# Optimization experiments

Hardware: AMD Instinct MI355X
Metric: run time of the kernel (lower is better)

The kernel has to match this reference:

```python
import jax, jax.numpy as jnp
import numpy as np

N = 100000   # nodes
E = 1600000  # edges (avg degree 16)
IN, HID, OUT = 128, 128, 64


def setup_inputs() -> dict:
    key = jax.random.key(0)
    k = jax.random.split(key, 6)
    feat = jax.random.normal(k[0], (N, IN), dtype=jnp.float32)
    src = jax.random.randint(k[1], (E,), 0, N)
    dst = jax.random.randint(k[2], (E,), 0, N)
    W1 = jax.random.normal(k[3], (IN, HID), dtype=jnp.float32) * (1.0 / np.sqrt(IN))
    b1 = jnp.zeros((HID,), dtype=jnp.float32)
    W2 = jax.random.normal(k[4], (HID, OUT), dtype=jnp.float32) * (1.0 / np.sqrt(HID))
    b2 = jnp.zeros((OUT,), dtype=jnp.float32)
    return {"feat": feat, "src": src, "dst": dst, "W1": W1, "b1": b1, "W2": W2, "b2": b2}


def _graph_conv(x, src, dst, c_src, c_dst, W, b):
    # DGL GraphConv, norm='both': D_dst^{-1/2} A (D_src^{-1/2} X W) + b
    # Apply W before the edge gather (mathematically identical, less edge traffic).
    h = (x * c_src[:, None]) @ W                      # [N, out]
    m = jax.ops.segment_sum(h[src], dst, num_segments=N)  # SpMM aggregate
    return m * c_dst[:, None] + b


def reference(feat, src, dst, W1, b1, W2, b2):
    ones = jnp.ones((src.shape[0],), dtype=feat.dtype)
    out_deg = jax.ops.segment_sum(ones, src, num_segments=N)
    in_deg = jax.ops.segment_sum(ones, dst, num_segments=N)
    c_src = jnp.clip(out_deg, 1.0, None) ** -0.5
    c_dst = jnp.clip(in_deg, 1.0, None) ** -0.5
    h = jax.nn.relu(_graph_conv(feat, src, dst, c_src, c_dst, W1, b1))
    h = _graph_conv(h, src, dst, c_src, c_dst, W2, b2)
    # dgl.mean_nodes over a single graph -> [1, OUT]
    return jnp.mean(h, axis=0, keepdims=True)
```

## Files before the change

### kernel.cpp

```cpp
#include <hip/hip_runtime.h>
#include <hip/hip_bf16.h>

#define FD 128
#define OD 64
#define SLOT 64
#define MAXNB 512
#define CHUNK 4096

typedef __hip_bfloat16 bf16;
typedef unsigned int u32;
typedef unsigned short u16;
typedef unsigned char u8;
typedef __attribute__((ext_vector_type(8))) short short8;
typedef __attribute__((ext_vector_type(4))) float f32x4;
typedef __attribute__((ext_vector_type(2))) float f32x2;

__device__ __forceinline__ float ldf(const float* p, size_t i) { return p[i]; }
__device__ __forceinline__ float ldf(const bf16* p, size_t i) { return __bfloat162float(p[i]); }
__device__ __forceinline__ float us2f(u16 u) {
    union { float f; u32 i; } w; w.i = ((u32)u) << 16; return w.f;
}
__device__ __forceinline__ u16 f2us(float f) {
    bf16 h = __float2bfloat16(f);
    return *reinterpret_cast<u16*>(&h);
}

__device__ __forceinline__ u32 f8e(float x) {
    union { float f; u32 i; } w; w.f = x;
    u32 s = (w.i >> 24) & 0x80u;
    float a = fabsf(x);
    if (a < 0.015625f) {
        u32 m = (u32)(int)rintf(a * 512.0f);
        return s | m;
    }
    if (a > 448.0f) a = 448.0f;
    w.f = a;
    u32 mag = w.i + 0x7FFFFu + ((w.i >> 20) & 1u);
    if (mag > 0x43E00000u) mag = 0x43E00000u;
    u32 e8 = (mag >> 23) - 120u;
    u32 m3 = (mag >> 20) & 7u;
    return s | (e8 << 3) | m3;
}
__device__ __forceinline__ float f8d(u32 b) {
    float v;
    if ((b & 0x78u) == 0u) {
        v = (float)(b & 7u) * 0x1p-9f;
    } else {
        union { u32 i; float f; } w;
        w.i = ((b & 0x7Fu) << 20) + 0x3C000000u;
        v = w.f;
    }
    return (b & 0x80u) ? -v : v;
}

__global__ void k_sniff(const u16* w1raw, unsigned* flag) {
    int t = threadIdx.x;
    int insane = 0;
    for (int i = t; i < 128; i += 64) {
        unsigned e = (w1raw[i] >> 7) & 0xFF;
        if (e != 0 && (e < 100 || e > 140)) insane++;
    }
    for (int o = 32; o > 0; o >>= 1) insane += __shfl_down(insane, o);
    if (t == 0) *flag = (insane > 16) ? 1u : 0u;
}

__global__ void k_wtF(const unsigned* __restrict__ flag,
                      const void* __restrict__ W1, const void* __restrict__ b1,
                      u16* __restrict__ W1T, float* __restrict__ b1f) {
    int t = blockIdx.x * 256 + threadIdx.x;
    int nn = t >> 7, k = t & 127;
    if (*flag == 0u) {
        W1T[t] = f2us(ldf((const bf16*)W1, (size_t)k * FD + nn));
        if (blockIdx.x == 0 && threadIdx.x < FD) b1f[threadIdx.x] = ldf((const bf16*)b1, threadIdx.x);
    } else {
        W1T[t] = f2us(ldf((const float*)W1, (size_t)k * FD + nn));
        if (blockIdx.x == 0 && threadIdx.x < FD) b1f[threadIdx.x] = ldf((const float*)b1, threadIdx.x);
    }
}

__global__ void k_f8F(const unsigned* __restrict__ flag,
                      const void* __restrict__ feat, const float* __restrict__ c_src,
                      u32* __restrict__ f8w, int N) {
    long wi = (long)blockIdx.x * 256 + threadIdx.x;
    long nw = (long)(N + 1) * 32;
    if (wi >= nw) return;
    int row = (int)(wi >> 5);
    if (row >= N) { f8w[wi] = 0u; return; }
    float cs = c_src[row];
    size_t b0 = (size_t)wi * 4;
    u32 pk;
    if (*flag == 0u) {
        const bf16* f = (const bf16*)feat;
        pk = f8e(cs * ldf(f, b0))       | (f8e(cs * ldf(f, b0 + 1)) << 8)
           | (f8e(cs * ldf(f, b0 + 2)) << 16) | (f8e(cs * ldf(f, b0 + 3)) << 24);
    } else {
        const float* f = (const float*)feat;
        pk = f8e(cs * ldf(f, b0))       | (f8e(cs * ldf(f, b0 + 1)) << 8)
           | (f8e(cs * ldf(f, b0 + 2)) << 16) | (f8e(cs * ldf(f, b0 + 3)) << 24);
    }
    f8w[wi] = pk;
}

__global__ __launch_bounds__(1024) void k_histC(const int* __restrict__ src,
                                                const int* __restrict__ dst,
                                                u32* __restrict__ cmT_d, u32* __restrict__ cmT_s,
                                                int E, int NB) {
    __shared__ u32 hd[MAXNB], hs[MAXNB];
    int t = threadIdx.x, blk = blockIdx.x;
    for (int i = t; i < NB; i += 1024) { hd[i] = 0; hs[i] = 0; }
    __syncthreads();
    long e0 = (long)blk * CHUNK;
    #pragma unroll
    for (int k = 0; k < CHUNK / 1024; k++) {
        long e = e0 + t + 1024L * k;
        if (e < E) {
            atomicAdd(&hd[((u32)dst[e]) >> 8], 1u);
            atomicAdd(&hs[((u32)src[e]) >> 8], 1u);
        }
    }
    __syncthreads();
    for (int i = t; i < NB; i += 1024) {
        cmT_d[(size_t)blk * NB + i] = hd[i];
        cmT_s[(size_t)blk * NB + i] = hs[i];
    }
}

__global__ __launch_bounds__(256) void k_colpre(u32* __restrict__ cmT_d, u32* __restrict__ cmT_s,
                                                u32* __restrict__ totd, u32* __restrict__ tots,
                                                int NB, int nchunk) {
    __shared__ u32 s[256];
    int bb = blockIdx.x;
    u32* cm = (bb < NB) ? cmT_d : cmT_s;
    u32* tot = (bb < NB) ? totd : tots;
    int b = (bb < NB) ? bb : bb - NB;
    int t = threadIdx.x;
    u32 carry = 0;
    for (int c0 = 0; c0 < nchunk; c0 += 256) {
        int c = c0 + t;
        u32 v = (c < nchunk) ? cm[(size_t)c * NB + b] : 0u;
        s[t] = v;
        __syncthreads();
        for (int o = 1; o < 256; o <<= 1) {
            u32 x = (t >= o) ? s[t - o] : 0u;
            __syncthreads();
            s[t] += x;
            __syncthreads();
        }
        if (c < nchunk) cm[(size_t)c * NB + b] = carry + s[t] - v;
        u32 btot = s[255];
        __syncthreads();
        carry += btot;
    }
    if (t == 0) tot[b] = carry;
}

__global__ void k_scanB(const u32* __restrict__ totd, const u32* __restrict__ tots,
                        u32* __restrict__ bstart_d, u32* __restrict__ bstart_s, int NB) {
    __shared__ u32 ts[1024];
    const u32* h = blockIdx.x ? tots : totd;
    u32* bs = blockIdx.x ? bstart_s : bstart_d;
    int t = threadIdx.x;
    int k = (NB + 1023) / 1024;
    int b0 = t * k;
    u32 s = 0;
    for (int i = 0; i < k; i++) { int b = b0 + i; if (b < NB) s += h[b]; }
    ts[t] = s;
    __syncthreads();
    for (int o = 1; o < 1024; o <<= 1) {
        u32 x = (t >= o) ? ts[t - o] : 0u;
        __syncthreads();
        ts[t] += x;
        __syncthreads();
    }
    u32 run = ts[t] - s;
    for (int i = 0; i < k; i++) {
        int b = b0 + i;
        if (b < NB) { bs[b] = run; run += h[b]; }
    }
}

__global__ __launch_bounds__(1024) void k_scat(const int* __restrict__ src,
                                               const int* __restrict__ dst,
                                               const u32* __restrict__ cmT_d,
                                               const u32* __restrict__ cmT_s,
                                               const u32* __restrict__ bstart_d,
                                               const u32* __restrict__ bstart_s,
                                               u32* __restrict__ pairs, u32* __restrict__ srcb,
                                               int E, int NB) {
    __shared__ u32 hd[MAXNB], hs[MAXNB];
    __shared__ u32 baseD[MAXNB], baseS[MAXNB];
    int t = threadIdx.x, blk = blockIdx.x;
    for (int i = t; i < NB; i += 1024) {
        hd[i] = 0; hs[i] = 0;
        baseD[i] = cmT_d[(size_t)blk * NB + i] + bstart_d[i];
        baseS[i] = cmT_s[(size_t)blk * NB + i] + bstart_s[i];
    }
    __syncthreads();
    long e0 = (long)blk * CHUNK;
    #pragma unroll
    for (int k = 0; k < CHUNK / 1024; k++) {
        long e = e0 + t + 1024L * k;
        if (e < E) {
            u32 s = (u32)src[e], d = (u32)dst[e];
            u32 rd = atomicAdd(&hd[d >> 8], 1u);
            u32 rs = atomicAdd(&hs[s >> 8], 1u);
            pairs[baseD[d >> 8] + rd] = ((d & 255u) << 24) | s;
            srcb [baseS[s >> 8] + rs] = ((s & 255u) << 24) | d;
        }
    }
}

__global__ __launch_bounds__(1024) void k_csr(const u32* __restrict__ pairs,
                                              const u32* __restrict__ bstart,
                                              const u32* __restrict__ bhist, u32* __restrict__ col,
                                              u32* __restrict__ cnt_d, float* __restrict__ c_dst,
                                              int N) {
    __shared__ u32 lc[256];
    int b = blockIdx.x, t = threadIdx.x;
    if (t < 256) lc[t] = 0;
    __syncthreads();
    u32 s0 = bstart[b], c = bhist[b];
    for (u32 i = t; i < c; i += 1024) {
        u32 pk = pairs[s0 + i];
        u32 local = pk >> 24;
        u32 r = atomicAdd(&lc[local], 1u);
        if (r < SLOT) col[(((size_t)b * 256 + local) << 6) + r] = pk & 0xFFFFFFu;
    }
    __syncthreads();
    if (t < 256) {
        int node = b * 256 + t;
        if (node < N) {
            cnt_d[node] = lc[t];
            c_dst[node] = rsqrtf(fmaxf((float)lc[t], 1.0f));
        }
    }
}

__global__ __launch_bounds__(1024) void k_cw(const u32* __restrict__ srcb,
                                             const u32* __restrict__ bstart,
                                             const u32* __restrict__ bhist,
                                             const float* __restrict__ c_dst,
                                             float* __restrict__ c_src, float* __restrict__ wprod,
                                             int N) {
    __shared__ u32 lc[256];
    __shared__ float acc[256];
    int b = blockIdx.x, t = threadIdx.x;
    if (t < 256) { lc[t] = 0; acc[t] = 0.0f; }
    __syncthreads();
    u32 s0 = bstart[b], c = bhist[b];
    for (u32 i = t; i < c; i += 1024) {
        u32 pk = srcb[s0 + i];
        atomicAdd(&lc[pk >> 24], 1u);
        atomicAdd(&acc[pk >> 24], c_dst[pk & 0xFFFFFFu]);
    }
    __syncthreads();
    if (t < 256) {
        int node = b * 256 + t;
        if (node < N) {
            float cs = rsqrtf(fmaxf((float)lc[t], 1.0f));
            c_src[node] = cs;
            wprod[node] = acc[t] * cs;
        }
    }
}

__global__ __launch_bounds__(256) void k_layer1a(const u8* __restrict__ f8,
                                                 const u16* __restrict__ W1T,
                                                 const float* __restrict__ b1f,
                                                 const float* __restrict__ c_dst,
                                                 const unsigned* __restrict__ cnt_d,
                                                 const unsigned* __restrict__ col,
                                                 u32* __restrict__ h1_32, int n) {
    __shared__ __align__(16) u16 xsb[64 * 144];
    __shared__ float b1l[FD];
    __shared__ float cdl[64];
    __shared__ unsigned degl[64];
    int t = threadIdx.x;
    int base = blockIdx.x * 64;

    if (t < FD) b1l[t] = b1f[t];
    if (t < 64) {
        int rr = base + t;
        unsigned cd = (rr < n) ? cnt_d[rr] : 0u;
        cdl[t] = (rr < n) ? c_dst[rr] : 0.0f;
        degl[t] = (cd < SLOT) ? cd : SLOT;
    }
    __syncthreads();

    int w = __builtin_amdgcn_readfirstlane(t >> 6);
    int l = t & 63;
    int m0 = w * 16;
    int q = l >> 4, lm = l & 15;
    int j0 = l * 2;
    unsigned zrow = (unsigned)n;

    for (int g = 0; g < 16; g++) {
        int loc = m0 + g;
        int node = base + loc;
        unsigned degv = degl[loc];
        size_t cb = ((size_t)node) << 6;
        float acc0 = 0.0f, acc1 = 0.0f;
        for (unsigned qq = 0; qq < degv; qq += 16) {
            unsigned lim = degv - qq;
            const unsigned* cp = col + cb + qq;
            uint4 P0 = *(const uint4*)(cp);
            uint4 P1 = *(const uint4*)(cp + 4);
            uint4 P2 = *(const uint4*)(cp + 8);
            uint4 P3 = *(const uint4*)(cp + 12);
            unsigned raw[16] = {P0.x, P0.y, P0.z, P0.w, P1.x, P1.y, P1.z, P1.w,
                                P2.x, P2.y, P2.z, P2.w, P3.x, P3.y, P3.z, P3.w};
            #pragma unroll
            for (int k = 0; k < 16; k++) {
                unsigned sk = __builtin_amdgcn_readfirstlane(raw[k]);
                sk = ((unsigned)k < lim) ? sk : zrow;
                u32 v = (u32)*(const u16*)(f8 + (((size_t)sk) << 7) + j0);
#if __has_builtin(__builtin_amdgcn_cvt_pk_f32_fp8)
                f32x2 dd = __builtin_amdgcn_cvt_pk_f32_fp8((int)v, false);
                acc0 += dd[0];
                acc1 += dd[1];
#else
                acc0 += f8d(v & 0xFFu);
                acc1 += f8d(v >> 8);
#endif
            }
        }
        u32 pk = ((u32)f2us(acc1) << 16) | (u32)f2us(acc0);
        *(u32*)&xsb[loc * 144 + j0] = pk;
    }

    short8 af[4];
    #pragma unroll
    for (int s = 0; s < 4; s++)
        af[s] = *(const short8*)&xsb[(m0 + lm) * 144 + s * 32 + q * 8];

    #pragma unroll 1
    for (int h2 = 0; h2 < 2; h2++) {
        #pragma unroll 1
        for (int tt = 0; tt < 4; tt++) {
            int nglob = h2 * 64 + tt * 16 + lm;
            f32x4 c = {0.0f, 0.0f, 0.0f, 0.0f};
            #pragma unroll
            for (int s = 0; s < 4; s++) {
                short8 bfr = *(const short8*)&W1T[(size_t)nglob * FD + s * 32 + q * 8];
                c = __builtin_amdgcn_mfma_f32_16x16x32_bf16(af[s], bfr, c, 0, 0, 0);
            }
            float bb = b1l[nglob];
            #pragma unroll
            for (int r = 0; r < 4; r++) {
                int loc = m0 + q * 4 + r;
                float hv = fmaxf(c[r] * cdl[loc] + bb, 0.0f);
                xsb[loc * 144 + nglob] = f2us(hv);
            }
        }
    }
    __syncthreads();

    #pragma unroll
    for (int i = 0; i < 16; i++) {
        int widx = t + 256 * i;
        int row = widx >> 6, cw = widx & 63;
        if (base + row < n)
            h1_32[((size_t)(base + row)) * 64 + cw] = *(const u32*)&xsb[row * 144 + cw * 2];
    }
}

__global__ __launch_bounds__(256) void k_l1b(const float* __restrict__ wprod,
                                             const u32* __restrict__ h1_32,
                                             float* __restrict__ accum128, int n) {
    __shared__ float part[4][FD];
    int t = threadIdx.x;
    int j2 = t & 63, sub = t >> 6;
    int per = (n + gridDim.x - 1) / gridDim.x;
    int b0 = blockIdx.x * per;
    int be = min(b0 + per, n);
    float a0 = 0.0f, a1 = 0.0f;
    for (int node = b0 + sub; node < be; node += 4) {
        float w = wprod[node];
        u32 v = h1_32[(size_t)node * 64 + j2];
        a0 += w * us2f((u16)(v & 0xffff));
        a1 += w * us2f((u16)(v >> 16));
    }
    part[sub][2 * j2]     = a0;
    part[sub][2 * j2 + 1] = a1;
    __syncthreads();
    if (t < FD)
        unsafeAtomicAdd(&accum128[t], part[0][t] + part[1][t] + part[2][t] + part[3][t]);
}

__global__ void k_finalF(const unsigned* __restrict__ flag,
                         const float* __restrict__ accum128,
                         const void* __restrict__ W2, const void* __restrict__ b2v,
                         void* __restrict__ out, float invN) {
    int j = threadIdx.x;
    float acc = 0.0f;
    if (*flag == 0u) {
        const bf16* w = (const bf16*)W2;
        for (int k = 0; k < FD; k++) acc += accum128[k] * ldf(w, (size_t)k * OD + j);
        ((bf16*)out)[j] = __float2bfloat16(acc * invN + ldf((const bf16*)b2v, j));
    } else {
        const float* w = (const float*)W2;
        for (int k = 0; k < FD; k++) acc += accum128[k] * ldf(w, (size_t)k * OD + j);
        ((float*)out)[j] = acc * invN + ldf((const float*)b2v, j);
    }
}

extern "C" void kernel_launch(void* const* d_in, const int* in_sizes, int n_in,
                              void* d_out, int out_size, void* d_ws, size_t ws_size,
                              hipStream_t stream) {
    const int* src = (const int*)d_in[1];
    const int* dst = (const int*)d_in[2];
    int N = in_sizes[0] / FD;
    int E = in_sizes[1];
    int NB = (N + 255) >> 8;
    int nchunk = (E + CHUNK - 1) / CHUNK;

    char* ws = (char*)d_ws;
    size_t o = 0;
    auto take = [&](size_t bytes) { size_t r = o; o = (o + bytes + 255) & ~(size_t)255; return r; };
    unsigned* flag     = (unsigned*)(ws + take(4096));
    float*    accum128 = (float*)   (ws + take(4096));
    u32*      totd     = (u32*)     (ws + take((size_t)NB * 4));
    u32*      tots     = (u32*)     (ws + take((size_t)NB * 4));
    u32*      bstart_d = (u32*)     (ws + take((size_t)NB * 4));
    u32*      bstart_s = (u32*)     (ws + take((size_t)NB * 4));
    float*    wprod    = (float*)   (ws + take((size_t)N * 4));
    float*    c_src    = (float*)   (ws + take((size_t)N * 4));
    float*    c_dst    = (float*)   (ws + take((size_t)N * 4));
    unsigned* cnt_d    = (unsigned*)(ws + take((size_t)N * 4));
    u16*      W1T      = (u16*)     (ws + take(FD * FD * 2));
    float*    b1f      = (float*)   (ws + take(FD * 4));
    u32*      cmT_d    = (u32*)     (ws + take((size_t)NB * nchunk * 4));
    u32*      cmT_s    = (u32*)     (ws + take((size_t)NB * nchunk * 4));
    size_t scrE = take((((size_t)E * 8) > ((size_t)N * 256)) ? ((size_t)E * 8) : ((size_t)N * 256));
    u32*      pairs    = (u32*)(ws + scrE);
    u32*      srcb     = pairs + E;
    u32*      h1_32    = (u32*)(ws + scrE);
    unsigned* col      = (unsigned*)(ws + take((size_t)N * SLOT * 4));
    u8*       f8       = (u8*)      (ws + take(((size_t)N + 1) * FD));

    hipMemsetAsync(accum128, 0, 4096, stream);

    k_sniff<<<1, 64, 0, stream>>>((const u16*)d_in[3], flag);
    k_wtF<<<64, 256, 0, stream>>>(flag, d_in[3], d_in[4], W1T, b1f);

    k_histC<<<nchunk, 1024, 0, stream>>>(src, dst, cmT_d, cmT_s, E, NB);
    k_colpre<<<2 * NB, 256, 0, stream>>>(cmT_d, cmT_s, totd, tots, NB, nchunk);
    k_scanB<<<2, 1024, 0, stream>>>(totd, tots, bstart_d, bstart_s, NB);
    k_scat<<<nchunk, 1024, 0, stream>>>(src, dst, cmT_d, cmT_s, bstart_d, bstart_s,
                                        pairs, srcb, E, NB);
    k_csr<<<NB, 1024, 0, stream>>>(pairs, bstart_d, totd, col, cnt_d, c_dst, N);
    k_cw<<<NB, 1024, 0, stream>>>(srcb, bstart_s, tots, c_dst, c_src, wprod, N);

    long nw8 = (long)(N + 1) * 32;
    k_f8F<<<(int)((nw8 + 255) / 256), 256, 0, stream>>>(flag, d_in[0], c_src, (u32*)f8, N);

    int gl1 = (N + 63) / 64;
    k_layer1a<<<gl1, 256, 0, stream>>>(f8, W1T, b1f, c_dst, cnt_d, col, h1_32, N);

    k_l1b<<<512, 256, 0, stream>>>(wprod, h1_32, accum128, N);

    float invN = 1.0f / (float)N;
    k_finalF<<<1, 64, 0, stream>>>(flag, accum128, d_in[5], d_in[6], d_out, invN);
}
```

Before: 264.0 us.

## Fuse preprocessing kernels and fold layer-1 reduction into the aggregation kernel

Merges the dtype-sniff, weight transpose and histogram kernels into one launch. The FP8 feature quantisation moves into the c_src kernel, and the accumulator memset into the block scan. The weighted column reduction that k_l1b did is now done inside k_layer1a with shuffles and a per-block atomic, so the bf16 h1 intermediate is never written to or read from global memory. This removes several launches and a full N×128 round trip. In exchange, the dtype sniff is recomputed in every block, and the block scan assumes NB ≤ 1024.

```diff
diff --git a/kernel.cpp b/kernel.cpp
--- a/kernel.cpp
+++ b/kernel.cpp
@@ -53,60 +53,42 @@
     return (b & 0x80u) ? -v : v;
 }
 
-__global__ void k_sniff(const u16* w1raw, unsigned* flag) {
-    int t = threadIdx.x;
-    int insane = 0;
-    for (int i = t; i < 128; i += 64) {
-        unsigned e = (w1raw[i] >> 7) & 0xFF;
-        if (e != 0 && (e < 100 || e > 140)) insane++;
-    }
-    for (int o = 32; o > 0; o >>= 1) insane += __shfl_down(insane, o);
-    if (t == 0) *flag = (insane > 16) ? 1u : 0u;
-}
-
-__global__ void k_wtF(const unsigned* __restrict__ flag,
-                      const void* __restrict__ W1, const void* __restrict__ b1,
-                      u16* __restrict__ W1T, float* __restrict__ b1f) {
-    int t = blockIdx.x * 256 + threadIdx.x;
-    int nn = t >> 7, k = t & 127;
-    if (*flag == 0u) {
-        W1T[t] = f2us(ldf((const bf16*)W1, (size_t)k * FD + nn));
-        if (blockIdx.x == 0 && threadIdx.x < FD) b1f[threadIdx.x] = ldf((const bf16*)b1, threadIdx.x);
-    } else {
-        W1T[t] = f2us(ldf((const float*)W1, (size_t)k * FD + nn));
-        if (blockIdx.x == 0 && threadIdx.x < FD) b1f[threadIdx.x] = ldf((const float*)b1, threadIdx.x);
-    }
-}
-
-__global__ void k_f8F(const unsigned* __restrict__ flag,
-                      const void* __restrict__ feat, const float* __restrict__ c_src,
-                      u32* __restrict__ f8w, int N) {
-    long wi = (long)blockIdx.x * 256 + threadIdx.x;
-    long nw = (long)(N + 1) * 32;
-    if (wi >= nw) return;
-    int row = (int)(wi >> 5);
-    if (row >= N) { f8w[wi] = 0u; return; }
-    float cs = c_src[row];
-    size_t b0 = (size_t)wi * 4;
-    u32 pk;
-    if (*flag == 0u) {
-        const bf16* f = (const bf16*)feat;
-        pk = f8e(cs * ldf(f, b0))       | (f8e(cs * ldf(f, b0 + 1)) << 8)
-           | (f8e(cs * ldf(f, b0 + 2)) << 16) | (f8e(cs * ldf(f, b0 + 3)) << 24);
-    } else {
-        const float* f = (const float*)feat;
-        pk = f8e(cs * ldf(f, b0))       | (f8e(cs * ldf(f, b0 + 1)) << 8)
-           | (f8e(cs * ldf(f, b0 + 2)) << 16) | (f8e(cs * ldf(f, b0 + 3)) << 24);
-    }
-    f8w[wi] = pk;
-}
-
-__global__ __launch_bounds__(1024) void k_histC(const int* __restrict__ src,
-                                                const int* __restrict__ dst,
-                                                u32* __restrict__ cmT_d, u32* __restrict__ cmT_s,
-                                                int E, int NB) {
-    __shared__ u32 hd[MAXNB], hs[MAXNB];
-    int t = threadIdx.x, blk = blockIdx.x;
+__device__ __forceinline__ u32 sniff(const u16* __restrict__ w1raw, u32* shflag) {
+    if (threadIdx.x < 64) {
+        int insane = 0;
+        for (int i = threadIdx.x; i < 128; i += 64) {
+            unsigned e = (w1raw[i] >> 7) & 0xFF;
+            if (e != 0 && (e < 100 || e > 140)) insane++;
+        }
+        for (int o = 32; o > 0; o >>= 1) insane += __shfl_down(insane, o);
+        if (threadIdx.x == 0) *shflag = (insane > 16) ? 1u : 0u;
+    }
+    __syncthreads();
+    return *shflag;
+}
+
+__global__ __launch_bounds__(1024) void k_hw(const int* __restrict__ src,
+                                             const int* __restrict__ dst,
+                                             const u16* __restrict__ w1raw,
+                                             const void* __restrict__ W1, const void* __restrict__ b1,
+                                             u16* __restrict__ W1T, float* __restrict__ b1f,
+                                             u32* __restrict__ cmT_d, u32* __restrict__ cmT_s,
+                                             int E, int NB) {
+    __shared__ u32 smem[1024];
+    __shared__ u32 flsh;
+    int t = threadIdx.x, blk = blockIdx.x, G = gridDim.x;
+    u32 fl = sniff(w1raw, &flsh);
+
+    for (long i = (long)blk * 1024 + t; i < FD * FD; i += (long)G * 1024) {
+        int nn = (int)(i >> 7), k = (int)(i & 127);
+        W1T[i] = fl ? f2us(ldf((const float*)W1, (size_t)k * FD + nn))
+                    : f2us(ldf((const bf16*)W1, (size_t)k * FD + nn));
+    }
+    if (blk == 0 && t < FD)
+        b1f[t] = fl ? ldf((const float*)b1, t) : ldf((const bf16*)b1, t);
+
+    u32* hd = smem;
+    u32* hs = smem + 512;
     for (int i = t; i < NB; i += 1024) { hd[i] = 0; hs[i] = 0; }
     __syncthreads();
     long e0 = (long)blk * CHUNK;
@@ -125,46 +107,45 @@
     }
 }
 
-__global__ __launch_bounds__(256) void k_colpre(u32* __restrict__ cmT_d, u32* __restrict__ cmT_s,
-                                                u32* __restrict__ totd, u32* __restrict__ tots,
-                                                int NB, int nchunk) {
-    __shared__ u32 s[256];
+__global__ __launch_bounds__(1024) void k_colpre(u32* __restrict__ cmT_d, u32* __restrict__ cmT_s,
+                                                 u32* __restrict__ totd, u32* __restrict__ tots,
+                                                 int NB, int nchunk) {
+    __shared__ u32 sS[1024];
     int bb = blockIdx.x;
-    u32* cm = (bb < NB) ? cmT_d : cmT_s;
+    u32* cm  = (bb < NB) ? cmT_d : cmT_s;
     u32* tot = (bb < NB) ? totd : tots;
     int b = (bb < NB) ? bb : bb - NB;
     int t = threadIdx.x;
     u32 carry = 0;
-    for (int c0 = 0; c0 < nchunk; c0 += 256) {
+    for (int c0 = 0; c0 < nchunk; c0 += 1024) {
         int c = c0 + t;
         u32 v = (c < nchunk) ? cm[(size_t)c * NB + b] : 0u;
-        s[t] = v;
+        sS[t] = v;
         __syncthreads();
-        for (int o = 1; o < 256; o <<= 1) {
-            u32 x = (t >= o) ? s[t - o] : 0u;
+        for (int o = 1; o < 1024; o <<= 1) {
+            u32 x = (t >= o) ? sS[t - o] : 0u;
             __syncthreads();
-            s[t] += x;
+            sS[t] += x;
             __syncthreads();
         }
-        if (c < nchunk) cm[(size_t)c * NB + b] = carry + s[t] - v;
-        u32 btot = s[255];
+        if (c < nchunk) cm[(size_t)c * NB + b] = carry + sS[t] - v;
+        u32 bt = sS[1023];
         __syncthreads();
-        carry += btot;
+        carry += bt;
     }
     if (t == 0) tot[b] = carry;
 }
 
 __global__ void k_scanB(const u32* __restrict__ totd, const u32* __restrict__ tots,
-                        u32* __restrict__ bstart_d, u32* __restrict__ bstart_s, int NB) {
+                        u32* __restrict__ bstart_d, u32* __restrict__ bstart_s,
+                        float* __restrict__ accum128, int NB) {
     __shared__ u32 ts[1024];
     const u32* h = blockIdx.x ? tots : totd;
     u32* bs = blockIdx.x ? bstart_s : bstart_d;
     int t = threadIdx.x;
-    int k = (NB + 1023) / 1024;
-    int b0 = t * k;
-    u32 s = 0;
-    for (int i = 0; i < k; i++) { int b = b0 + i; if (b < NB) s += h[b]; }
-    ts[t] = s;
+    if (blockIdx.x == 0 && t < FD) accum128[t] = 0.0f;
+    u32 v = (t < NB) ? h[t] : 0u;
+    ts[t] = v;
     __syncthreads();
     for (int o = 1; o < 1024; o <<= 1) {
         u32 x = (t >= o) ? ts[t - o] : 0u;
@@ -172,11 +153,7 @@
         ts[t] += x;
         __syncthreads();
     }
-    u32 run = ts[t] - s;
-    for (int i = 0; i < k; i++) {
-        int b = b0 + i;
-        if (b < NB) { bs[b] = run; run += h[b]; }
-    }
+    if (t < NB) bs[t] = ts[t] - v;
 }
 
 __global__ __launch_bounds__(1024) void k_scat(const int* __restrict__ src,
@@ -236,32 +213,59 @@
     }
 }
 
-__global__ __launch_bounds__(1024) void k_cw(const u32* __restrict__ srcb,
-                                             const u32* __restrict__ bstart,
-                                             const u32* __restrict__ bhist,
-                                             const float* __restrict__ c_dst,
-                                             float* __restrict__ c_src, float* __restrict__ wprod,
-                                             int N) {
+__global__ __launch_bounds__(1024) void k_cwf8(const u32* __restrict__ srcb,
+                                               const u32* __restrict__ bstart,
+                                               const u32* __restrict__ bhist,
+                                               const float* __restrict__ c_dst,
+                                               float* __restrict__ c_src, float* __restrict__ wprod,
+                                               const u16* __restrict__ w1raw,
+                                               const void* __restrict__ feat,
+                                               u32* __restrict__ f8w, int N) {
     __shared__ u32 lc[256];
-    __shared__ float acc[256];
+    __shared__ float accF[256];
+    __shared__ float csl[256];
+    __shared__ u32 flsh;
     int b = blockIdx.x, t = threadIdx.x;
-    if (t < 256) { lc[t] = 0; acc[t] = 0.0f; }
+    u32 fl = sniff(w1raw, &flsh);
+    if (t < 256) { lc[t] = 0; accF[t] = 0.0f; }
     __syncthreads();
     u32 s0 = bstart[b], c = bhist[b];
     for (u32 i = t; i < c; i += 1024) {
         u32 pk = srcb[s0 + i];
         atomicAdd(&lc[pk >> 24], 1u);
-        atomicAdd(&acc[pk >> 24], c_dst[pk & 0xFFFFFFu]);
+        atomicAdd(&accF[pk >> 24], c_dst[pk & 0xFFFFFFu]);
     }
     __syncthreads();
     if (t < 256) {
         int node = b * 256 + t;
+        float cs = 0.0f;
         if (node < N) {
-            float cs = rsqrtf(fmaxf((float)lc[t], 1.0f));
+            cs = rsqrtf(fmaxf((float)lc[t], 1.0f));
             c_src[node] = cs;
-            wprod[node] = acc[t] * cs;
-        }
-    }
+            wprod[node] = accF[t] * cs;
+        }
+        csl[t] = cs;
+    }
+    __syncthreads();
+    for (int wi = t; wi < 256 * 32; wi += 1024) {
+        int row = wi >> 5;
+        int node = b * 256 + row;
+        if (node >= N) continue;
+        float cs = csl[row];
+        size_t b0 = (size_t)node * FD + (size_t)(wi & 31) * 4;
+        u32 pk;
+        if (fl == 0u) {
+            const bf16* f = (const bf16*)feat;
+            pk = f8e(cs * ldf(f, b0))       | (f8e(cs * ldf(f, b0 + 1)) << 8)
+               | (f8e(cs * ldf(f, b0 + 2)) << 16) | (f8e(cs * ldf(f, b0 + 3)) << 24);
+        } else {
+            const float* f = (const float*)feat;
+            pk = f8e(cs * ldf(f, b0))       | (f8e(cs * ldf(f, b0 + 1)) << 8)
+               | (f8e(cs * ldf(f, b0 + 2)) << 16) | (f8e(cs * ldf(f, b0 + 3)) << 24);
+        }
+        f8w[(size_t)node * 32 + (wi & 31)] = pk;
+    }
+    if (b == 0 && t < 32) f8w[(size_t)N * 32 + t] = 0u;
 }
 
 __global__ __launch_bounds__(256) void k_layer1a(const u8* __restrict__ f8,
@@ -270,11 +274,13 @@
                                                  const float* __restrict__ c_dst,
                                                  const unsigned* __restrict__ cnt_d,
                                                  const unsigned* __restrict__ col,
-                                                 u32* __restrict__ h1_32, int n) {
+                                                 const float* __restrict__ wprod,
+                                                 float* __restrict__ accum128, int n) {
     __shared__ __align__(16) u16 xsb[64 * 144];
     __shared__ float b1l[FD];
-    __shared__ float cdl[64];
+    __shared__ float cdl[64], wpl[64];
     __shared__ unsigned degl[64];
+    __shared__ float part[4][FD];
     int t = threadIdx.x;
     int base = blockIdx.x * 64;
 
@@ -283,6 +289,7 @@
         int rr = base + t;
         unsigned cd = (rr < n) ? cnt_d[rr] : 0u;
         cdl[t] = (rr < n) ? c_dst[rr] : 0.0f;
+        wpl[t] = (rr < n) ? wprod[rr] : 0.0f;
         degl[t] = (cd < SLOT) ? cd : SLOT;
     }
     __syncthreads();
@@ -345,55 +352,32 @@
                 c = __builtin_amdgcn_mfma_f32_16x16x32_bf16(af[s], bfr, c, 0, 0, 0);
             }
             float bb = b1l[nglob];
+            float ps = 0.0f;
             #pragma unroll
             for (int r = 0; r < 4; r++) {
                 int loc = m0 + q * 4 + r;
                 float hv = fmaxf(c[r] * cdl[loc] + bb, 0.0f);
-                xsb[loc * 144 + nglob] = f2us(hv);
+                ps += wpl[loc] * hv;
             }
-        }
-    }
-    __syncthreads();
-
-    #pragma unroll
-    for (int i = 0; i < 16; i++) {
-        int widx = t + 256 * i;
-        int row = widx >> 6, cw = widx & 63;
-        if (base + row < n)
-            h1_32[((size_t)(base + row)) * 64 + cw] = *(const u32*)&xsb[row * 144 + cw * 2];
-    }
-}
-
-__global__ __launch_bounds__(256) void k_l1b(const float* __restrict__ wprod,
-                                             const u32* __restrict__ h1_32,
-                                             float* __restrict__ accum128, int n) {
-    __shared__ float part[4][FD];
-    int t = threadIdx.x;
-    int j2 = t & 63, sub = t >> 6;
-    int per = (n + gridDim.x - 1) / gridDim.x;
-    int b0 = blockIdx.x * per;
-    int be = min(b0 + per, n);
-    float a0 = 0.0f, a1 = 0.0f;
-    for (int node = b0 + sub; node < be; node += 4) {
-        float w = wprod[node];
-        u32 v = h1_32[(size_t)node * 64 + j2];
-        a0 += w * us2f((u16)(v & 0xffff));
-        a1 += w * us2f((u16)(v >> 16));
-    }
-    part[sub][2 * j2]     = a0;
-    part[sub][2 * j2 + 1] = a1;
+            ps += __shfl_down(ps, 32);
+            ps += __shfl_down(ps, 16);
+            if (l < 16) part[w][nglob] = ps;
+        }
+    }
     __syncthreads();
     if (t < FD)
         unsafeAtomicAdd(&accum128[t], part[0][t] + part[1][t] + part[2][t] + part[3][t]);
 }
 
-__global__ void k_finalF(const unsigned* __restrict__ flag,
+__global__ void k_finalF(const u16* __restrict__ w1raw,
                          const float* __restrict__ accum128,
                          const void* __restrict__ W2, const void* __restrict__ b2v,
                          void* __restrict__ out, float invN) {
+    __shared__ u32 flsh;
+    u32 fl = sniff(w1raw, &flsh);
     int j = threadIdx.x;
     float acc = 0.0f;
-    if (*flag == 0u) {
+    if (fl == 0u) {
         const bf16* w = (const bf16*)W2;
         for (int k = 0; k < FD; k++) acc += accum128[k] * ldf(w, (size_t)k * OD + j);
         ((bf16*)out)[j] = __float2bfloat16(acc * invN + ldf((const bf16*)b2v, j));
@@ -417,8 +401,7 @@
     char* ws = (char*)d_ws;
     size_t o = 0;
     auto take = [&](size_t bytes) { size_t r = o; o = (o + bytes + 255) & ~(size_t)255; return r; };
-    unsigned* flag     = (unsigned*)(ws + take(4096));
-    float*    accum128 = (float*)   (ws + take(4096));
+    float*    accum128 = (float*)   (ws + take(FD * 4));
     u32*      totd     = (u32*)     (ws + take((size_t)NB * 4));
     u32*      tots     = (u32*)     (ws + take((size_t)NB * 4));
     u32*      bstart_d = (u32*)     (ws + take((size_t)NB * 4));
@@ -431,34 +414,26 @@
     float*    b1f      = (float*)   (ws + take(FD * 4));
     u32*      cmT_d    = (u32*)     (ws + take((size_t)NB * nchunk * 4));
     u32*      cmT_s    = (u32*)     (ws + take((size_t)NB * nchunk * 4));
-    size_t scrE = take((((size_t)E * 8) > ((size_t)N * 256)) ? ((size_t)E * 8) : ((size_t)N * 256));
-    u32*      pairs    = (u32*)(ws + scrE);
-    u32*      srcb     = pairs + E;
-    u32*      h1_32    = (u32*)(ws + scrE);
-    unsigned* col      = (unsigned*)(ws + take((size_t)N * SLOT * 4));
+    u32*      pairs    = (u32*)     (ws + take((size_t)E * 4));
+    u32*      srcb     = (u32*)     (ws + take((size_t)E * 4));
+    u32*      col      = (u32*)     (ws + take((size_t)N * SLOT * 4));
     u8*       f8       = (u8*)      (ws + take(((size_t)N + 1) * FD));
 
-    hipMemsetAsync(accum128, 0, 4096, stream);
-
-    k_sniff<<<1, 64, 0, stream>>>((const u16*)d_in[3], flag);
-    k_wtF<<<64, 256, 0, stream>>>(flag, d_in[3], d_in[4], W1T, b1f);
-
-    k_histC<<<nchunk, 1024, 0, stream>>>(src, dst, cmT_d, cmT_s, E, NB);
-    k_colpre<<<2 * NB, 256, 0, stream>>>(cmT_d, cmT_s, totd, tots, NB, nchunk);
-    k_scanB<<<2, 1024, 0, stream>>>(totd, tots, bstart_d, bstart_s, NB);
+    const u16* w1raw = (const u16*)d_in[3];
+
+    k_hw<<<nchunk, 1024, 0, stream>>>(src, dst, w1raw, d_in[3], d_in[4], W1T, b1f,
+                                      cmT_d, cmT_s, E, NB);
+    k_colpre<<<2 * NB, 1024, 0, stream>>>(cmT_d, cmT_s, totd, tots, NB, nchunk);
+    k_scanB<<<2, 1024, 0, stream>>>(totd, tots, bstart_d, bstart_s, accum128, NB);
     k_scat<<<nchunk, 1024, 0, stream>>>(src, dst, cmT_d, cmT_s, bstart_d, bstart_s,
                                         pairs, srcb, E, NB);
     k_csr<<<NB, 1024, 0, stream>>>(pairs, bstart_d, totd, col, cnt_d, c_dst, N);
-    k_cw<<<NB, 1024, 0, stream>>>(srcb, bstart_s, tots, c_dst, c_src, wprod, N);
-
-    long nw8 = (long)(N + 1) * 32;
-    k_f8F<<<(int)((nw8 + 255) / 256), 256, 0, stream>>>(flag, d_in[0], c_src, (u32*)f8, N);
+    k_cwf8<<<NB, 1024, 0, stream>>>(srcb, bstart_s, tots, c_dst, c_src, wprod,
+                                    w1raw, d_in[0], (u32*)f8, N);
 
     int gl1 = (N + 63) / 64;
-    k_layer1a<<<gl1, 256, 0, stream>>>(f8, W1T, b1f, c_dst, cnt_d, col, h1_32, N);
-
-    k_l1b<<<512, 256, 0, stream>>>(wprod, h1_32, accum128, N);
+    k_layer1a<<<gl1, 256, 0, stream>>>(f8, W1T, b1f, c_dst, cnt_d, col, wprod, accum128, N);
 
     float invN = 1.0f / (float)N;
-    k_finalF<<<1, 64, 0, stream>>>(flag, accum128, d_in[5], d_in[6], d_out, invN);
-}
+    k_finalF<<<1, 64, 0, stream>>>(w1raw, accum128, d_in[5], d_in[6], d_out, invN);
+}
```

New measurement: 267.7 us. Within noise of the previous version (+1.4%).
